# Performance work log

Hardware: AMD Instinct MI355X
Metric: run time of the kernel (lower is better)

Reference implementation:

```python
import jax, jax.numpy as jnp
import numpy as np

BN_EPS = 1e-5

def setup_inputs() -> dict:
    key = jax.random.key(0)
    k_x, k_e, k_w, k_g = jax.random.split(key, 4)
    N, E, C_in, C_out = 100000, 1600000, 64, 64
    x = jax.random.normal(k_x, (N, C_in), dtype=jnp.float32)
    edge_index = jax.random.randint(k_e, (2, E), 0, N, dtype=jnp.int64)
    # GCNConv params: linear weight (no bias in lin; bias added after aggregation)
    lim = 1.0 / np.sqrt(C_in)
    W = jax.random.uniform(k_w, (C_in, C_out), minval=-lim, maxval=lim, dtype=jnp.float32)
    bias = jnp.zeros((C_out,), dtype=jnp.float32)
    # BatchNorm1d affine params
    gamma = jnp.ones((C_out,), dtype=jnp.float32)
    beta = jnp.zeros((C_out,), dtype=jnp.float32)
    return {"x": x, "edge_index": edge_index, "W": W, "bias": bias,
            "gamma": gamma, "beta": beta}

def reference(x, edge_index, W, bias, gamma, beta):
    # GCNConv (PyG defaults): add self-loops (weight 1), symmetric normalization,
    # out[dst] += norm(e) * (x @ W)[src], then + bias.
    N = x.shape[0]
    loop = jnp.arange(N, dtype=edge_index.dtype)
    src = jnp.concatenate([edge_index[0], loop])   # [E+N] message sources
    dst = jnp.concatenate([edge_index[1], loop])   # [E+N] message targets
    ew = jnp.ones(src.shape[0], dtype=x.dtype)     # edge_weight=None -> ones
    deg = jax.ops.segment_sum(ew, dst, num_segments=N)          # [N]
    dinv = jnp.where(deg > 0, jax.lax.rsqrt(deg), 0.0)
    norm = dinv[src] * ew * dinv[dst]              # [E+N]
    h = x @ W                                      # [N, C_out]
    msg = h[src] * norm[:, None]                   # gather + scale  [E+N, C_out]
    out = jax.ops.segment_sum(msg, dst, num_segments=N) + bias   # scatter-add
    # BatchNorm1d (training-mode batch stats, biased variance), then ReLU.
    mean = out.mean(axis=0)
    var = out.var(axis=0)
    out = (out - mean) * jax.lax.rsqrt(var + BN_EPS) * gamma + beta
    out = jnp.maximum(out, 0.0)
    # Dropout evaluated as identity (deterministic reference).
    return out
```

## Files before the change

### kernel.cpp

```cpp
#include <hip/hip_runtime.h>
#include <hip/hip_bf16.h>

#ifndef BN_EPS
#define BN_EPS 1e-5f
#endif


#define CAP2 3072

__device__ __forceinline__ unsigned short f2bf(float f) {
    unsigned u = __float_as_uint(f);
    u += 0x7FFF + ((u >> 16) & 1);
    return (unsigned short)(u >> 16);
}
__device__ __forceinline__ float bf2f(unsigned v) {
    return __uint_as_float(v << 16);
}

__global__ __launch_bounds__(256) void k_pre(const int* __restrict__ src,
                                             const int* __restrict__ dst,
                                             int* __restrict__ cnt2,
                                             unsigned* __restrict__ binned,
                                             unsigned* __restrict__ ybz,
                                             int E, int SUB) {
    __shared__ int h2[1024];
    __shared__ int gbase[784];
    __shared__ int hcur[784];
    __shared__ unsigned lout[4096];
    __shared__ unsigned short lb[4096];
    int tid = threadIdx.x;
    if (blockIdx.x == 0) {
        if (tid < 32) ybz[tid] = 0u;
    }
    int c0 = blockIdx.x * 4096;
    if (c0 >= E) return;
    int cnt = min(4096, E - c0);
    for (int i = tid; i < 1024; i += 256) h2[i] = 0;
    __syncthreads();
    for (int i = tid; i < cnt; i += 256)
        atomicAdd(&h2[dst[c0 + i] >> 7], 1);
    __syncthreads();
    for (int off = 1; off < 1024; off <<= 1) {
        int t0 = tid, t1 = tid + 256, t2 = tid + 512, t3 = tid + 768;
        int a0 = (t0 >= off) ? h2[t0 - off] : 0;
        int a1 = (t1 >= off) ? h2[t1 - off] : 0;
        int a2 = (t2 >= off) ? h2[t2 - off] : 0;
        int a3 = (t3 >= off) ? h2[t3 - off] : 0;
        __syncthreads();
        h2[t0] += a0; h2[t1] += a1; h2[t2] += a2; h2[t3] += a3;
        __syncthreads();
    }
    for (int s2 = tid; s2 < SUB; s2 += 256) {
        int prev = s2 ? h2[s2 - 1] : 0;
        int v = h2[s2] - prev;
        hcur[s2] = prev;
        if (v > 0) gbase[s2] = atomicAdd(&cnt2[s2], v);
    }
    __syncthreads();
    for (int i = tid; i < cnt; i += 256) {
        int d = dst[c0 + i];
        int s = src[c0 + i];
        int sb = d >> 7;
        unsigned packed = (unsigned)s | ((unsigned)(d & 127) << 17);
        int p = atomicAdd(&hcur[sb], 1);
        lout[p] = packed;
        lb[p] = (unsigned short)sb;
    }
    __syncthreads();
    for (int i = tid; i < cnt; i += 256) {
        int sb = lb[i];
        int hx = sb ? h2[sb - 1] : 0;
        binned[(size_t)sb * CAP2 + gbase[sb] + (i - hx)] = lout[i];
    }
}

__global__ __launch_bounds__(256) void k_csr(const int* __restrict__ cnt2,
                                             unsigned* __restrict__ binned,
                                             int* __restrict__ deg,
                                             float* __restrict__ dinv,
                                             int* __restrict__ offs,
                                             int N) {
    __shared__ int hist[128], lbase[128], lcur[128];
    __shared__ unsigned win[CAP2];
    int s = blockIdx.x;
    int tid = threadIdx.x;
    int cnt = cnt2[s];
    unsigned* bb = binned + (size_t)s * CAP2;
    for (int j = tid; j < cnt; j += 256) win[j] = bb[j];
    if (tid < 128) { hist[tid] = 0; lcur[tid] = 0; }
    __syncthreads();
    for (int j = tid; j < cnt; j += 256)
        atomicAdd(&hist[win[j] >> 17], 1);
    __syncthreads();
    if (tid == 0) {
        int acc = 0;
        for (int k = 0; k < 128; k++) { lbase[k] = acc; acc += hist[k]; }
    }
    __syncthreads();
    if (tid < 128) {
        int n = (s << 7) + tid;
        if (n < N) {
            deg[n] = hist[tid];
            dinv[n] = rsqrtf((float)(hist[tid] + 1));
            offs[n] = s * CAP2 + lbase[tid];
        }
    }
    __syncthreads();
    for (int j = tid; j < cnt; j += 256) {
        unsigned e = win[j];
        int ld = e >> 17;
        bb[lbase[ld] + atomicAdd(&lcur[ld], 1)] = e & 0x1FFFFu;
    }
}

__global__ __launch_bounds__(256) void k_proj(const float* __restrict__ x,
                                              const float* __restrict__ W,
                                              const float* __restrict__ dinv,
                                              unsigned short* __restrict__ yb,
                                              int N) {
    __shared__ unsigned tile[64 * 32];
    __shared__ float sdv[64];
    int t = threadIdx.x;
    int lane = t & 63;
    int w = t >> 6;
    int r0 = blockIdx.x * 64;
    const float4* gp = (const float4*)(x + (size_t)r0 * 64);
#pragma unroll
    for (int i = 0; i < 4; i++) {
        int idx = t + 256 * i;
        int n = r0 + (idx >> 4);
        float4 v = {0.f, 0.f, 0.f, 0.f};
        if (n < N) v = gp[idx];
        unsigned lo = (unsigned)f2bf(v.x) | ((unsigned)f2bf(v.y) << 16);
        unsigned hi = (unsigned)f2bf(v.z) | ((unsigned)f2bf(v.w) << 16);
        tile[(idx >> 4) * 32 + (idx & 15) * 2] = lo;
        tile[(idx >> 4) * 32 + (idx & 15) * 2 + 1] = hi;
    }
    if (t < 64) {
        int n = r0 + t;
        sdv[t] = (n < N) ? dinv[n] : 0.f;
    }
    float wcol[64];
#pragma unroll
    for (int k = 0; k < 64; k++) wcol[k] = W[k * 64 + lane];
    __syncthreads();

#pragma unroll
    for (int rr = 0; rr < 16; rr += 2) {
        int lr0 = w * 16 + rr;
        int n0 = r0 + lr0;
        if (n0 >= N) break;
        const unsigned* row0 = tile + lr0 * 32;
        const unsigned* row1 = row0 + 32;
        float o0 = 0.f, o1 = 0.f;
#pragma unroll
        for (int kp = 0; kp < 32; kp++) {
            unsigned u0 = row0[kp], u1 = row1[kp];
            o0 = fmaf(bf2f(u0 & 0xFFFFu), wcol[2 * kp], o0);
            o0 = fmaf(bf2f(u0 >> 16), wcol[2 * kp + 1], o0);
            o1 = fmaf(bf2f(u1 & 0xFFFFu), wcol[2 * kp], o1);
            o1 = fmaf(bf2f(u1 >> 16), wcol[2 * kp + 1], o1);
        }
        yb[(size_t)n0 * 64 + lane] = f2bf(o0 * sdv[lr0]);
        if (n0 + 1 < N)
            yb[(size_t)(n0 + 1) * 64 + lane] = f2bf(o1 * sdv[lr0 + 1]);
    }
}

__global__ __launch_bounds__(256) void k_agg(const int* __restrict__ offs,
                                             const int* __restrict__ deg,
                                             const int* __restrict__ csr,
                                             const unsigned short* __restrict__ yb,
                                             const float* __restrict__ dinv,
                                             unsigned* __restrict__ yagg,
                                             float* __restrict__ stats_p, int N) {
    __shared__ float red[512];
    int tid = threadIdx.x;
    int lane = tid & 63;
    int p = lane & 31;
    int h = lane >> 5;
    int w = tid >> 6;
    int wid = (blockIdx.x * 256 + tid) >> 6;
    int nw = (gridDim.x * 256) >> 6;
    const unsigned* xw = (const unsigned*)yb;

    float psx = 0.f, psy = 0.f, pqx = 0.f, pqy = 0.f;
    for (int n = wid; n < N; n += nw) {
        float dn = dinv[n];
        unsigned sv = xw[(size_t)n * 32 + p];
        float accx = (h == 0) ? bf2f(sv & 0xFFFFu) : 0.f;
        float accy = (h == 0) ? bf2f(sv >> 16) : 0.f;
        int j0 = offs[n];
        int j1 = j0 + deg[n];
        for (int jb = j0; jb < j1; jb += 64) {
            int cnt = min(64, j1 - jb);
            int idx = N;
            if (lane < cnt) idx = csr[jb + lane];
            for (int j = 0; j < cnt; j += 16) {
                int s0 = __shfl(idx, j + 0 + h),  s1 = __shfl(idx, j + 2 + h);
                int s2 = __shfl(idx, j + 4 + h),  s3 = __shfl(idx, j + 6 + h);
                int s4 = __shfl(idx, j + 8 + h),  s5 = __shfl(idx, j + 10 + h);
                int s6 = __shfl(idx, j + 12 + h), s7 = __shfl(idx, j + 14 + h);
                unsigned v0 = xw[(size_t)s0 * 32 + p];
                unsigned v1 = xw[(size_t)s1 * 32 + p];
                unsigned v2 = xw[(size_t)s2 * 32 + p];
                unsigned v3 = xw[(size_t)s3 * 32 + p];
                unsigned v4 = xw[(size_t)s4 * 32 + p];
                unsigned v5 = xw[(size_t)s5 * 32 + p];
                unsigned v6 = xw[(size_t)s6 * 32 + p];
                unsigned v7 = xw[(size_t)s7 * 32 + p];
                accx += bf2f(v0 & 0xFFFFu); accy += bf2f(v0 >> 16);
                accx += bf2f(v1 & 0xFFFFu); accy += bf2f(v1 >> 16);
                accx += bf2f(v2 & 0xFFFFu); accy += bf2f(v2 >> 16);
                accx += bf2f(v3 & 0xFFFFu); accy += bf2f(v3 >> 16);
                accx += bf2f(v4 & 0xFFFFu); accy += bf2f(v4 >> 16);
                accx += bf2f(v5 & 0xFFFFu); accy += bf2f(v5 >> 16);
                accx += bf2f(v6 & 0xFFFFu); accy += bf2f(v6 >> 16);
                accx += bf2f(v7 & 0xFFFFu); accy += bf2f(v7 >> 16);
            }
        }
        accx += __shfl_xor(accx, 32);
        accy += __shfl_xor(accy, 32);
        float ox = accx * dn, oy = accy * dn;
        if (h == 0) {
            unsigned o = (unsigned)f2bf(ox) | ((unsigned)f2bf(oy) << 16);
            yagg[(size_t)n * 32 + p] = o;
            psx += ox; pqx = fmaf(ox, ox, pqx);
            psy += oy; pqy = fmaf(oy, oy, pqy);
        }
    }
    if (h == 0) {
        red[w * 32 + p] = psx;
        red[128 + w * 32 + p] = psy;
        red[256 + w * 32 + p] = pqx;
        red[384 + w * 32 + p] = pqy;
    }
    __syncthreads();
    float* sp = stats_p + (blockIdx.x & 63) * 128;
    if (tid < 64) {
        int c = tid, pp = c >> 1, odd = c & 1;
        float* b = red + odd * 128;
        atomicAdd(&sp[c], b[pp] + b[32 + pp] + b[64 + pp] + b[96 + pp]);
    } else if (tid < 128) {
        int c = tid - 64, pp = c >> 1, odd = c & 1;
        float* b = red + 256 + odd * 128;
        atomicAdd(&sp[64 + c], b[pp] + b[32 + pp] + b[64 + pp] + b[96 + pp]);
    }
}

__global__ __launch_bounds__(256) void k_bn(const unsigned* __restrict__ yagg,
                                            const float* __restrict__ stats_p,
                                            const float* __restrict__ gamma,
                                            const float* __restrict__ beta,
                                            float* __restrict__ out, int N,
                                            float invN) {
    __shared__ float ssl[128];
    int t = threadIdx.x;
    if (t < 64) {
        float s = 0.f, q = 0.f;
        for (int j = 0; j < 64; j++) {
            s += stats_p[j * 128 + t];
            q += stats_p[j * 128 + 64 + t];
        }
        float mean = s * invN;
        float var = q * invN - mean * mean;
        float sc = gamma[t] * rsqrtf(var + BN_EPS);
        ssl[t] = sc;
        ssl[64 + t] = beta[t] - mean * sc;
    }
    __syncthreads();
    int total = N * 32;
    for (int i = blockIdx.x * 256 + t; i < total; i += gridDim.x * 256) {
        unsigned u = yagg[i];
        int p = i & 31;
        float2 o;
        o.x = fmaxf(fmaf(bf2f(u & 0xFFFFu), ssl[2 * p], ssl[64 + 2 * p]), 0.f);
        o.y = fmaxf(fmaf(bf2f(u >> 16), ssl[2 * p + 1], ssl[64 + 2 * p + 1]), 0.f);
        ((float2*)out)[i] = o;
    }
}

extern "C" void kernel_launch(void* const* d_in, const int* in_sizes, int n_in,
                              void* d_out, int out_size, void* d_ws, size_t ws_size,
                              hipStream_t stream) {
    const float* x = (const float*)d_in[0];
    const int* ei = (const int*)d_in[1];
    const float* W = (const float*)d_in[2];
    const float* gamma = (const float*)d_in[4];
    const float* beta = (const float*)d_in[5];
    float* out = (float*)d_out;

    const int N = in_sizes[0] / 64;
    const int E = in_sizes[1] / 2;
    const int* src = ei;
    const int* dst = ei + E;
    const int SUB = (N + 127) >> 7;

    char* ws = (char*)d_ws;
    size_t o = 0;
    int* cnt2 = (int*)(ws + o); o += 4096;
    float* stats_p = (float*)(ws + o); o += 32768;
    int* deg = (int*)(ws + o); o += (size_t)4 * N;
    int* offs = (int*)(ws + o); o += (size_t)4 * N;
    float* dinv = (float*)(ws + o); o += (size_t)4 * N;
    unsigned short* yb = (unsigned short*)(ws + o); o += (size_t)128 * (N + 1);
    unsigned* yagg = (unsigned*)(ws + o); o += (size_t)128 * N;
    unsigned* binned = (unsigned*)(ws + o); o += (size_t)4 * SUB * CAP2;

    hipMemsetAsync(ws, 0, 36864, stream);

    const int EB = (E + 4095) / 4096;
    const int PB = (N + 63) / 64;
    k_pre<<<EB, 256, 0, stream>>>(src, dst, cnt2, binned,
                                  (unsigned*)(yb + (size_t)N * 64), E, SUB);
    k_csr<<<SUB, 256, 0, stream>>>(cnt2, binned, deg, dinv, offs, N);
    k_proj<<<PB, 256, 0, stream>>>(x, W, dinv, yb, N);
    k_agg<<<2048, 256, 0, stream>>>(offs, deg, (const int*)binned, yb, dinv,
                                    yagg, stats_p, N);
    k_bn<<<1024, 256, 0, stream>>>(yagg, stats_p, gamma, beta, out, N,
                                   1.0f / (float)N);
}
```

Before: 190.6 us.

## Fuse projection into edge-binning kernel and apply dinv scaling in CSR pass

The projection x@W now runs as extra blocks inside the edge-binning kernel, so it overlaps with the edge histogram work instead of waiting behind the CSR kernel. The dinv row scaling, which needs degrees, moves into the CSR kernel, which rescales its 128-node slice of the bf16 projected features in place. This removes one kernel launch and the serial dependency of the projection on dinv. In exchange it adds a second read-modify-write pass over the projected features and rounds to bf16 twice, which slightly changes numerics.

```diff
diff --git a/kernel.cpp b/kernel.cpp
--- a/kernel.cpp
+++ b/kernel.cpp
@@ -19,20 +19,67 @@
 
 __global__ __launch_bounds__(256) void k_pre(const int* __restrict__ src,
                                              const int* __restrict__ dst,
+                                             const float* __restrict__ x,
+                                             const float* __restrict__ W,
                                              int* __restrict__ cnt2,
                                              unsigned* __restrict__ binned,
+                                             unsigned short* __restrict__ yb,
                                              unsigned* __restrict__ ybz,
-                                             int E, int SUB) {
-    __shared__ int h2[1024];
-    __shared__ int gbase[784];
-    __shared__ int hcur[784];
-    __shared__ unsigned lout[4096];
-    __shared__ unsigned short lb[4096];
+                                             int E, int SUB, int EB, int N) {
+    __shared__ __align__(16) char smem[34944];
     int tid = threadIdx.x;
-    if (blockIdx.x == 0) {
+    int bid = blockIdx.x;
+    if (bid == 0) {
         if (tid < 32) ybz[tid] = 0u;
     }
-    int c0 = blockIdx.x * 4096;
+    if (bid >= EB) {
+        unsigned* tile = (unsigned*)smem;
+        int lane = tid & 63;
+        int w = tid >> 6;
+        int r0 = (bid - EB) * 64;
+        const float4* gp = (const float4*)(x + (size_t)r0 * 64);
+#pragma unroll
+        for (int i = 0; i < 4; i++) {
+            int idx = tid + 256 * i;
+            int n = r0 + (idx >> 4);
+            float4 v = {0.f, 0.f, 0.f, 0.f};
+            if (n < N) v = gp[idx];
+            unsigned lo = (unsigned)f2bf(v.x) | ((unsigned)f2bf(v.y) << 16);
+            unsigned hi = (unsigned)f2bf(v.z) | ((unsigned)f2bf(v.w) << 16);
+            tile[(idx >> 4) * 32 + (idx & 15) * 2] = lo;
+            tile[(idx >> 4) * 32 + (idx & 15) * 2 + 1] = hi;
+        }
+        float wcol[64];
+#pragma unroll
+        for (int k = 0; k < 64; k++) wcol[k] = W[k * 64 + lane];
+        __syncthreads();
+#pragma unroll
+        for (int rr = 0; rr < 16; rr += 2) {
+            int lr0 = w * 16 + rr;
+            int n0 = r0 + lr0;
+            if (n0 >= N) break;
+            const unsigned* row0 = tile + lr0 * 32;
+            const unsigned* row1 = row0 + 32;
+            float o0 = 0.f, o1 = 0.f;
+#pragma unroll
+            for (int kp = 0; kp < 32; kp++) {
+                unsigned u0 = row0[kp], u1 = row1[kp];
+                o0 = fmaf(bf2f(u0 & 0xFFFFu), wcol[2 * kp], o0);
+                o0 = fmaf(bf2f(u0 >> 16), wcol[2 * kp + 1], o0);
+                o1 = fmaf(bf2f(u1 & 0xFFFFu), wcol[2 * kp], o1);
+                o1 = fmaf(bf2f(u1 >> 16), wcol[2 * kp + 1], o1);
+            }
+            yb[(size_t)n0 * 64 + lane] = f2bf(o0);
+            if (n0 + 1 < N) yb[(size_t)(n0 + 1) * 64 + lane] = f2bf(o1);
+        }
+        return;
+    }
+    int* h2 = (int*)smem;
+    int* gbase = (int*)(smem + 4096);
+    int* hcur = (int*)(smem + 7232);
+    unsigned* lout = (unsigned*)(smem + 10368);
+    unsigned short* lb = (unsigned short*)(smem + 26752);
+    int c0 = bid * 4096;
     if (c0 >= E) return;
     int cnt = min(4096, E - c0);
     for (int i = tid; i < 1024; i += 256) h2[i] = 0;
@@ -79,8 +126,10 @@
                                              int* __restrict__ deg,
                                              float* __restrict__ dinv,
                                              int* __restrict__ offs,
+                                             unsigned* __restrict__ ybw,
                                              int N) {
     __shared__ int hist[128], lbase[128], lcur[128];
+    __shared__ float sdv[128];
     __shared__ unsigned win[CAP2];
     int s = blockIdx.x;
     int tid = threadIdx.x;
@@ -99,9 +148,11 @@
     __syncthreads();
     if (tid < 128) {
         int n = (s << 7) + tid;
+        float dn = rsqrtf((float)(hist[tid] + 1));
+        sdv[tid] = dn;
         if (n < N) {
             deg[n] = hist[tid];
-            dinv[n] = rsqrtf((float)(hist[tid] + 1));
+            dinv[n] = dn;
             offs[n] = s * CAP2 + lbase[tid];
         }
     }
@@ -111,59 +162,16 @@
         int ld = e >> 17;
         bb[lbase[ld] + atomicAdd(&lcur[ld], 1)] = e & 0x1FFFFu;
     }
-}
-
-__global__ __launch_bounds__(256) void k_proj(const float* __restrict__ x,
-                                              const float* __restrict__ W,
-                                              const float* __restrict__ dinv,
-                                              unsigned short* __restrict__ yb,
-                                              int N) {
-    __shared__ unsigned tile[64 * 32];
-    __shared__ float sdv[64];
-    int t = threadIdx.x;
-    int lane = t & 63;
-    int w = t >> 6;
-    int r0 = blockIdx.x * 64;
-    const float4* gp = (const float4*)(x + (size_t)r0 * 64);
-#pragma unroll
-    for (int i = 0; i < 4; i++) {
-        int idx = t + 256 * i;
-        int n = r0 + (idx >> 4);
-        float4 v = {0.f, 0.f, 0.f, 0.f};
-        if (n < N) v = gp[idx];
-        unsigned lo = (unsigned)f2bf(v.x) | ((unsigned)f2bf(v.y) << 16);
-        unsigned hi = (unsigned)f2bf(v.z) | ((unsigned)f2bf(v.w) << 16);
-        tile[(idx >> 4) * 32 + (idx & 15) * 2] = lo;
-        tile[(idx >> 4) * 32 + (idx & 15) * 2 + 1] = hi;
-    }
-    if (t < 64) {
-        int n = r0 + t;
-        sdv[t] = (n < N) ? dinv[n] : 0.f;
-    }
-    float wcol[64];
-#pragma unroll
-    for (int k = 0; k < 64; k++) wcol[k] = W[k * 64 + lane];
-    __syncthreads();
-
-#pragma unroll
-    for (int rr = 0; rr < 16; rr += 2) {
-        int lr0 = w * 16 + rr;
-        int n0 = r0 + lr0;
-        if (n0 >= N) break;
-        const unsigned* row0 = tile + lr0 * 32;
-        const unsigned* row1 = row0 + 32;
-        float o0 = 0.f, o1 = 0.f;
-#pragma unroll
-        for (int kp = 0; kp < 32; kp++) {
-            unsigned u0 = row0[kp], u1 = row1[kp];
-            o0 = fmaf(bf2f(u0 & 0xFFFFu), wcol[2 * kp], o0);
-            o0 = fmaf(bf2f(u0 >> 16), wcol[2 * kp + 1], o0);
-            o1 = fmaf(bf2f(u1 & 0xFFFFu), wcol[2 * kp], o1);
-            o1 = fmaf(bf2f(u1 >> 16), wcol[2 * kp + 1], o1);
-        }
-        yb[(size_t)n0 * 64 + lane] = f2bf(o0 * sdv[lr0]);
-        if (n0 + 1 < N)
-            yb[(size_t)(n0 + 1) * 64 + lane] = f2bf(o1 * sdv[lr0 + 1]);
+    unsigned* yrow = ybw + (size_t)(s << 7) * 32;
+    for (int i = tid; i < 4096; i += 256) {
+        int n = (s << 7) + (i >> 5);
+        if (n < N) {
+            float dn = sdv[i >> 5];
+            unsigned u = yrow[i];
+            unsigned lo = f2bf(bf2f(u & 0xFFFFu) * dn);
+            unsigned hi = f2bf(bf2f(u >> 16) * dn);
+            yrow[i] = lo | (hi << 16);
+        }
     }
 }
 
@@ -311,10 +319,11 @@
 
     const int EB = (E + 4095) / 4096;
     const int PB = (N + 63) / 64;
-    k_pre<<<EB, 256, 0, stream>>>(src, dst, cnt2, binned,
-                                  (unsigned*)(yb + (size_t)N * 64), E, SUB);
-    k_csr<<<SUB, 256, 0, stream>>>(cnt2, binned, deg, dinv, offs, N);
-    k_proj<<<PB, 256, 0, stream>>>(x, W, dinv, yb, N);
+    k_pre<<<EB + PB, 256, 0, stream>>>(src, dst, x, W, cnt2, binned, yb,
+                                       (unsigned*)(yb + (size_t)N * 64),
+                                       E, SUB, EB, N);
+    k_csr<<<SUB, 256, 0, stream>>>(cnt2, binned, deg, dinv, offs,
+                                   (unsigned*)yb, N);
     k_agg<<<2048, 256, 0, stream>>>(offs, deg, (const int*)binned, yb, dinv,
                                     yagg, stats_p, N);
     k_bn<<<1024, 256, 0, stream>>>(yagg, stats_p, gamma, beta, out, N,
```

Result: faster. 186.2 us (-2.3%).
